# Performance work log

Hardware: AMD Instinct MI355X
Metric: run time of the kernel (lower is better)

## Reference

```python
import jax, jax.numpy as jnp
import numpy as np

S, O, J, B = 16, 8, 32, 4096
HID, OUT_HID = 240, 512
P1, P2 = 0.5, 0.65  # Bayesian (concrete) dropout probabilities, mid of [0.5, 0.8]


def setup_inputs() -> dict:
    key = jax.random.key(0)
    ks = jax.random.split(key, 20)
    sc = 0.05
    return {
        "y_t": jax.random.normal(ks[0], (B, O), jnp.float32),
        "x_filtered_prev": jax.random.normal(ks[1], (B, S), jnp.float32),
        "F": jax.random.normal(ks[2], (S, S), jnp.float32) * sc,
        "H": jax.random.normal(ks[3], (O, S), jnp.float32) * sc,
        "W_fc_in": jax.random.normal(ks[4], (HID, 2 * S + 2 * O), jnp.float32) * sc,
        "b_fc_in": jax.random.normal(ks[5], (HID,), jnp.float32) * sc,
        "W_ih": jax.random.normal(ks[6], (3 * HID, HID), jnp.float32) * sc,
        "W_hh": jax.random.normal(ks[7], (3 * HID, HID), jnp.float32) * sc,
        "b_ih": jax.random.normal(ks[8], (3 * HID,), jnp.float32) * sc,
        "b_hh": jax.random.normal(ks[9], (3 * HID,), jnp.float32) * sc,
        "W_out1": jax.random.normal(ks[10], (OUT_HID, HID), jnp.float32) * sc,
        "b_out1": jax.random.normal(ks[11], (OUT_HID,), jnp.float32) * sc,
        "W_out2": jax.random.normal(ks[12], (S * O, OUT_HID), jnp.float32) * sc,
        "b_out2": jax.random.normal(ks[13], (S * O,), jnp.float32) * sc,
        "h_init": jax.random.normal(ks[14], (HID,), jnp.float32),
        "u1": jax.random.uniform(ks[15], (J, B, HID), jnp.float32),
        "u2": jax.random.uniform(ks[16], (J, B, OUT_HID), jnp.float32),
    }


def reference(y_t, x_filtered_prev, F, H, W_fc_in, b_fc_in, W_ih, W_hh, b_ih,
              b_hh, W_out1, b_out1, W_out2, b_out2, h_init, u1, u2):
    # --- first step of step_StateBayesianKalmanNet, fully batched over (J, B) ---
    x_pred = x_filtered_prev @ F.T                 # f(x): [B,S]
    y_pred = x_pred @ H.T                          # h(x): [B,O]
    state_inno = x_filtered_prev - x_pred          # x_filt_prev - x_pred_prev
    innovation = y_t - y_pred
    diff_state = jnp.zeros_like(x_filtered_prev)   # first step: x_prev - x_prev_prev = 0
    diff_obs = y_t - y_pred                        # y_prev = h(x_pred) on first step

    feats = jnp.concatenate([state_inno, innovation, diff_state, diff_obs], -1)  # [B,48]
    x_in = jax.nn.relu(feats @ W_fc_in.T + b_fc_in)                              # [B,HID]
    mask1 = (u1 > P1).astype(x_in.dtype) / (1.0 - P1)                            # [J,B,HID]
    x_in = x_in[None] * mask1                                                    # Bayesian dropout sample j

    # single GRU cell step (torch gate order r,z,n), h_prev = h_init broadcast
    gx = x_in @ W_ih.T + b_ih                                                    # [J,B,3H]
    gh = h_init @ W_hh.T + b_hh                                                  # [3H]
    xr, xz, xn = jnp.split(gx, 3, axis=-1)
    hr, hz, hn = jnp.split(gh, 3, axis=-1)
    r = jax.nn.sigmoid(xr + hr)
    z = jax.nn.sigmoid(xz + hz)
    n = jnp.tanh(xn + r * hn)
    h_new = (1.0 - z) * n + z * h_init                                           # [J,B,HID]

    o1 = jax.nn.relu(h_new @ W_out1.T + b_out1)                                  # [J,B,OUT_HID]
    mask2 = (u2 > P2).astype(o1.dtype) / (1.0 - P2)
    o1 = o1 * mask2
    K_vec = o1 @ W_out2.T + b_out2                                               # [J,B,S*O]
    K = K_vec.reshape(J, B, S, O)

    correction = jnp.einsum('jbso,bo->jbs', K, innovation)
    x_filt = x_pred[None] + correction                                           # [J,B,S]
    ensemble = jnp.transpose(x_filt, (1, 0, 2))                                  # [B,J,S]
    final_x = ensemble.mean(axis=1)
    final_P_diag = ensemble.var(axis=1, ddof=1)                                  # torch unbiased var

    # concrete-dropout regularization (entropy of the two dropout gates, mean over J)
    reg = -(P1 * jnp.log(P1) + (1 - P1) * jnp.log(1 - P1)) \
          - (P2 * jnp.log(P2) + (1 - P2) * jnp.log(1 - P2))
    reg = jnp.asarray(reg, final_x.dtype)

    return final_x, final_P_diag, reg, ensemble
```

## Files before the change

kernel.cpp:

```cpp
#include <hip/hip_runtime.h>
#include <hip/hip_bf16.h>
#include <math.h>

#define S_DIM 16
#define O_DIM 8
#define J_DIM 32
#define B_DIM 4096
#define HID 240
#define OHID 512

typedef __attribute__((ext_vector_type(8))) short bf16x8;
typedef __attribute__((ext_vector_type(4))) float f32x4;
#define MFMA16(a,b,c) __builtin_amdgcn_mfma_f32_16x16x32_bf16((a),(b),(c),0,0,0)

#define WS_XPRED   0
#define WS_INNO    (WS_XPRED + B_DIM*S_DIM)
#define WS_FEATS   (WS_INNO + B_DIM*O_DIM)
#define WS_XIN0    (WS_FEATS + B_DIM*48)
#define WS_GH      (WS_XIN0 + B_DIM*HID)
#define WS_WB_OFF  ((WS_GH + 960) * 4)

#define OUT_X      0
#define OUT_P      (B_DIM*S_DIM)
#define OUT_REG    (2*B_DIM*S_DIM)
#define OUT_ENS    (2*B_DIM*S_DIM + 1)

__global__ void k_aux_pre(const float* __restrict__ W_ih, const float* __restrict__ W_hh,
                          const float* __restrict__ b_ih, const float* __restrict__ b_hh,
                          const float* __restrict__ h_init,
                          const float* __restrict__ W_o1, const float* __restrict__ W_o2,
                          __hip_bfloat16* __restrict__ Wihb, __hip_bfloat16* __restrict__ Wo1b,
                          __hip_bfloat16* __restrict__ Wo2b, float* __restrict__ ghb,
                          const float* __restrict__ y, const float* __restrict__ xprev,
                          const float* __restrict__ F, const float* __restrict__ Hm,
                          float* __restrict__ x_pred, float* __restrict__ inno,
                          float* __restrict__ feats)
{
    __shared__ float sF[256], sH[128];
    const int tid = threadIdx.x;
    if (blockIdx.x < 1536) {
        int t = blockIdx.x * 256 + tid;
        if (t < 768*256) {
            int n = t >> 8, k = t & 255;
            float v = (n < 720 && k < 240) ? W_ih[n*240 + k] : 0.0f;
            Wihb[t] = __float2bfloat16(v);
        } else if (t < 768*256 + 512*256) {
            int u = t - 768*256;
            int n = u >> 8, k = u & 255;
            float v = (k < 240) ? W_o1[n*240 + k] : 0.0f;
            Wo1b[u] = __float2bfloat16(v);
        } else if (t < 768*256 + 512*256 + 128*512) {
            int u = t - 768*256 - 512*256;
            Wo2b[u] = __float2bfloat16(W_o2[u]);
        }
        if (t < 720) {
            float a = b_hh[t];
            const float* wr = W_hh + t*240;
            for (int k = 0; k < 240; k++) a = fmaf(h_init[k], wr[k], a);
            if (t < 480) {
                ghb[t] = b_ih[t] + a;
            } else {
                ghb[t] = b_ih[t];
                ghb[t + 240] = a;
            }
        }
        return;
    }
    sF[tid] = F[tid];
    if (tid < 128) sH[tid] = Hm[tid];
    __syncthreads();
    int b = (blockIdx.x - 1536) * 256 + tid;
    float xf[16], xp[16], inn[8];
    #pragma unroll
    for (int s = 0; s < 16; s++) xf[s] = xprev[b*16 + s];
    #pragma unroll
    for (int s = 0; s < 16; s++) {
        float a = 0.f;
        #pragma unroll
        for (int k = 0; k < 16; k++) a = fmaf(xf[k], sF[s*16 + k], a);
        xp[s] = a;
    }
    #pragma unroll
    for (int o = 0; o < 8; o++) {
        float a = 0.f;
        #pragma unroll
        for (int k = 0; k < 16; k++) a = fmaf(xp[k], sH[o*16 + k], a);
        inn[o] = y[b*8 + o] - a;
    }
    #pragma unroll
    for (int s = 0; s < 16; s++) x_pred[b*16 + s] = xp[s];
    #pragma unroll
    for (int o = 0; o < 8; o++) inno[b*8 + o] = inn[o];
    float* fb = feats + b*48;
    #pragma unroll
    for (int s = 0; s < 16; s++) fb[s] = xf[s] - xp[s];
    #pragma unroll
    for (int o = 0; o < 8; o++) fb[16 + o] = inn[o];
    #pragma unroll
    for (int s = 0; s < 16; s++) fb[24 + s] = 0.f;
    #pragma unroll
    for (int o = 0; o < 8; o++) fb[40 + o] = inn[o];
}

__global__ void k_pre_b(const float* __restrict__ feats, const float* __restrict__ Wfc,
                        const float* __restrict__ bfc, float* __restrict__ x_in0)
{
    int t = blockIdx.x * 256 + threadIdx.x;
    int b = t / 240, h = t - b*240;
    const float* fb = feats + b*48;
    const float* wr = Wfc + h*48;
    float a = bfc[h];
    #pragma unroll
    for (int k = 0; k < 48; k += 4) {
        const float4 f4 = *(const float4*)&fb[k];
        const float4 w4 = *(const float4*)&wr[k];
        a = fmaf(f4.x, w4.x, fmaf(f4.y, w4.y, fmaf(f4.z, w4.z, fmaf(f4.w, w4.w, a))));
    }
    x_in0[t] = fmaxf(a, 0.f);
}

#define XS_STRIDE 264
#define O1_STRIDE 520

__global__ __launch_bounds__(256, 4) void k_main(
    const float* __restrict__ x_in0, const float* __restrict__ u1,
    const float* __restrict__ u2,
    const __hip_bfloat16* __restrict__ Wihb, const float* __restrict__ ghb,
    const float* __restrict__ h_init,
    const __hip_bfloat16* __restrict__ Wo1b, const float* __restrict__ b_out1,
    const __hip_bfloat16* __restrict__ Wo2b, const float* __restrict__ b_out2,
    const float* __restrict__ x_pred, const float* __restrict__ inno,
    float* __restrict__ ens)
{
    __shared__ __align__(16) char smem[38912];
    __hip_bfloat16* Xs  = (__hip_bfloat16*)smem;
    __hip_bfloat16* Hs  = (__hip_bfloat16*)(smem + 16896);
    __hip_bfloat16* O1s = (__hip_bfloat16*)smem;
    unsigned int* Mbits = (unsigned int*)(smem + 33792);
    float* XPs   = (float*)(smem + 35840);
    float* InnoS = (float*)(smem + 37888);

    const int tid = threadIdx.x;
    const int j  = blockIdx.x >> 7;
    const int b0 = (blockIdx.x & 127) << 5;

    {
        const float4* u2t = (const float4*)(u2 + ((size_t)(j*B_DIM + b0) << 9));
        const int sh = (tid & 7) * 4;
        #pragma unroll
        for (int it = 0; it < 16; ++it) {
            float4 q = u2t[tid + 256*it];
            unsigned int nib = (q.x > 0.65f ? 1u : 0u) | (q.y > 0.65f ? 2u : 0u)
                             | (q.z > 0.65f ? 4u : 0u) | (q.w > 0.65f ? 8u : 0u);
            unsigned int v = nib << sh;
            v |= __shfl_xor(v, 1);
            v |= __shfl_xor(v, 2);
            v |= __shfl_xor(v, 4);
            if ((tid & 7) == 0) Mbits[(tid >> 3) + 32*it] = v;
        }
    }

    {
        const float4* xt = (const float4*)(x_in0 + b0*240);
        const float4* ut = (const float4*)(u1 + (size_t)(j*B_DIM + b0)*240);
        #pragma unroll
        for (int it = 0; it < 8; ++it) {
            int idx = tid + 256*it;
            if (idx < 1920) {
                float4 xv = xt[idx];
                float4 uv = ut[idx];
                int flat = idx * 4;
                int i = flat / 240;
                int h = flat - i*240;
                __hip_bfloat16 o[4];
                o[0] = __float2bfloat16(uv.x > 0.5f ? 2.0f*xv.x : 0.0f);
                o[1] = __float2bfloat16(uv.y > 0.5f ? 2.0f*xv.y : 0.0f);
                o[2] = __float2bfloat16(uv.z > 0.5f ? 2.0f*xv.z : 0.0f);
                o[3] = __float2bfloat16(uv.w > 0.5f ? 2.0f*xv.w : 0.0f);
                *(uint2*)&Xs[i*XS_STRIDE + h] = *(const uint2*)o;
            }
        }
    }
    if (tid < 128) {
        int row = tid >> 2, c = 240 + ((tid & 3) << 2);
        uint2 z = {0u, 0u};
        *(uint2*)&Xs[row*XS_STRIDE + c] = z;
        *(uint2*)&Hs[row*XS_STRIDE + c] = z;
    }
    XPs[tid]       = x_pred[b0*16 + tid];
    XPs[tid + 256] = x_pred[b0*16 + tid + 256];
    InnoS[tid]     = inno[b0*8 + tid];
    __syncthreads();

    const int wave = tid >> 6;
    const int l15  = tid & 15;
    const int quad = (tid >> 4) & 3;
    const f32x4 zero4 = {0.f, 0.f, 0.f, 0.f};

    #pragma unroll 1
    for (int it = 0; it < 4; ++it) {
        f32x4 aR[2], aZ[2], aN[2];
        #pragma unroll
        for (int m = 0; m < 2; ++m) { aR[m] = zero4; aZ[m] = zero4; aN[m] = zero4; }

        const int nrow = (wave + 4*it)*16 + l15;
        const __hip_bfloat16* wr = Wihb + nrow*256;
        #pragma unroll
        for (int ks = 0; ks < 8; ++ks) {
            const int ko = ks*32 + quad*8;
            bf16x8 a0 = *(const bf16x8*)&Xs[l15*XS_STRIDE + ko];
            bf16x8 a1 = *(const bf16x8*)&Xs[(16 + l15)*XS_STRIDE + ko];
            bf16x8 br = *(const bf16x8*)&wr[ko];
            bf16x8 bz = *(const bf16x8*)&wr[240*256 + ko];
            bf16x8 bn = *(const bf16x8*)&wr[480*256 + ko];
            aR[0] = MFMA16(a0, br, aR[0]);
            aR[1] = MFMA16(a1, br, aR[1]);
            aZ[0] = MFMA16(a0, bz, aZ[0]);
            aZ[1] = MFMA16(a1, bz, aZ[1]);
            aN[0] = MFMA16(a0, bn, aN[0]);
            aN[1] = MFMA16(a1, bn, aN[1]);
        }
        const int t = wave + 4*it;
        if (t < 15) {
            const int h = t*16 + l15;
            const float add_r = ghb[h],       add_z = ghb[240 + h];
            const float add_n = ghb[480 + h], mul_n = ghb[720 + h];
            const float hi = h_init[h];
            #pragma unroll
            for (int m = 0; m < 2; ++m)
                #pragma unroll
                for (int r = 0; r < 4; ++r) {
                    const int row = m*16 + quad*4 + r;
                    float rg = 1.0f/(1.0f + expf(-(aR[m][r] + add_r)));
                    float zg = 1.0f/(1.0f + expf(-(aZ[m][r] + add_z)));
                    float ng = tanhf(aN[m][r] + add_n + rg*mul_n);
                    Hs[row*XS_STRIDE + h] = __float2bfloat16((1.0f - zg)*ng + zg*hi);
                }
        }
    }
    __syncthreads();

    {
        f32x4 acc2[8][2];
        #pragma unroll
        for (int it = 0; it < 8; it++) { acc2[it][0] = zero4; acc2[it][1] = zero4; }

        #pragma unroll
        for (int ks = 0; ks < 8; ++ks) {
            const int ko = ks*32 + quad*8;
            bf16x8 a0 = *(const bf16x8*)&Hs[l15*XS_STRIDE + ko];
            bf16x8 a1 = *(const bf16x8*)&Hs[(16 + l15)*XS_STRIDE + ko];
            #pragma unroll
            for (int it = 0; it < 8; ++it) {
                const int n = (wave*8 + it)*16 + l15;
                bf16x8 b = *(const bf16x8*)&Wo1b[n*256 + ko];
                acc2[it][0] = MFMA16(a0, b, acc2[it][0]);
                acc2[it][1] = MFMA16(a1, b, acc2[it][1]);
            }
        }
        __syncthreads();
        const float inv35 = 1.0f/0.35f;
        #pragma unroll
        for (int it = 0; it < 8; ++it) {
            const int n = (wave*8 + it)*16 + l15;
            const float bb = b_out1[n];
            const int wbase = wave*4 + (it >> 1);
            const int bitpos = ((it & 1) << 4) | l15;
            #pragma unroll
            for (int m = 0; m < 2; ++m)
                #pragma unroll
                for (int r = 0; r < 4; ++r) {
                    const int row = m*16 + quad*4 + r;
                    unsigned int mw = Mbits[row*16 + wbase];
                    float o = fmaxf(acc2[it][m][r] + bb, 0.0f);
                    o = ((mw >> bitpos) & 1u) ? o*inv35 : 0.0f;
                    O1s[row*O1_STRIDE + n] = __float2bfloat16(o);
                }
        }
    }
    __syncthreads();

    {
        f32x4 acc3[2][2];
        #pragma unroll
        for (int it = 0; it < 2; ++it) {
            const int n = (wave*2 + it)*16 + l15;
            const float bo = b_out2[n];
            f32x4 v = {bo, bo, bo, bo};
            acc3[it][0] = v; acc3[it][1] = v;
        }
        #pragma unroll
        for (int ks = 0; ks < 16; ++ks) {
            const int ko = ks*32 + quad*8;
            bf16x8 a0 = *(const bf16x8*)&O1s[l15*O1_STRIDE + ko];
            bf16x8 a1 = *(const bf16x8*)&O1s[(16 + l15)*O1_STRIDE + ko];
            #pragma unroll
            for (int it = 0; it < 2; ++it) {
                const int n = (wave*2 + it)*16 + l15;
                bf16x8 b = *(const bf16x8*)&Wo2b[n*512 + ko];
                acc3[it][0] = MFMA16(a0, b, acc3[it][0]);
                acc3[it][1] = MFMA16(a1, b, acc3[it][1]);
            }
        }
        #pragma unroll
        for (int it = 0; it < 2; ++it) {
            const int n = (wave*2 + it)*16 + l15;
            const int s = n >> 3, o = n & 7;
            #pragma unroll
            for (int m = 0; m < 2; ++m)
                #pragma unroll
                for (int r = 0; r < 4; ++r) {
                    const int row = m*16 + quad*4 + r;
                    float v = acc3[it][m][r] * InnoS[row*8 + o];
                    v += __shfl_xor(v, 1);
                    v += __shfl_xor(v, 2);
                    v += __shfl_xor(v, 4);
                    if (o == 0)
                        ens[((b0 + row)*J_DIM + j)*16 + s] = XPs[row*16 + s] + v;
                }
        }
    }
}

__global__ void k_final(const float* __restrict__ ens, float* __restrict__ out)
{
    int t = blockIdx.x * 256 + threadIdx.x;
    int b = t >> 4, s = t & 15;
    float v[32];
    #pragma unroll
    for (int jj = 0; jj < 32; jj++) v[jj] = ens[(b*32 + jj)*16 + s];
    float m = 0.f;
    #pragma unroll
    for (int jj = 0; jj < 32; jj++) m += v[jj];
    m *= (1.0f/32.0f);
    float var = 0.f;
    #pragma unroll
    for (int jj = 0; jj < 32; jj++) { float d = v[jj] - m; var = fmaf(d, d, var); }
    var *= (1.0f/31.0f);
    out[OUT_X + t] = m;
    out[OUT_P + t] = var;
    if (t == 0) out[OUT_REG] = 1.3405938195945778f;
}

extern "C" void kernel_launch(void* const* d_in, const int* in_sizes, int n_in,
                              void* d_out, int out_size, void* d_ws, size_t ws_size,
                              hipStream_t stream)
{
    (void)in_sizes; (void)n_in; (void)out_size; (void)ws_size;
    const float* y_t    = (const float*)d_in[0];
    const float* xprev  = (const float*)d_in[1];
    const float* F      = (const float*)d_in[2];
    const float* Hm     = (const float*)d_in[3];
    const float* Wfc    = (const float*)d_in[4];
    const float* bfc    = (const float*)d_in[5];
    const float* W_ih   = (const float*)d_in[6];
    const float* W_hh   = (const float*)d_in[7];
    const float* b_ih   = (const float*)d_in[8];
    const float* b_hh   = (const float*)d_in[9];
    const float* W_o1   = (const float*)d_in[10];
    const float* b_o1   = (const float*)d_in[11];
    const float* W_o2   = (const float*)d_in[12];
    const float* b_o2   = (const float*)d_in[13];
    const float* h_init = (const float*)d_in[14];
    const float* u1     = (const float*)d_in[15];
    const float* u2     = (const float*)d_in[16];

    float* out = (float*)d_out;
    float* ws  = (float*)d_ws;
    float* x_pred = ws + WS_XPRED;
    float* inno   = ws + WS_INNO;
    float* feats  = ws + WS_FEATS;
    float* x_in0  = ws + WS_XIN0;
    float* ghb    = ws + WS_GH;
    __hip_bfloat16* Wihb = (__hip_bfloat16*)((char*)d_ws + WS_WB_OFF);
    __hip_bfloat16* Wo1b = Wihb + 768*256;
    __hip_bfloat16* Wo2b = Wo1b + 512*256;
    float* ens    = out + OUT_ENS;

    k_aux_pre<<<dim3(1552), dim3(256), 0, stream>>>(W_ih, W_hh, b_ih, b_hh, h_init,
                                                    W_o1, W_o2, Wihb, Wo1b, Wo2b, ghb,
                                                    y_t, xprev, F, Hm, x_pred, inno, feats);
    k_pre_b<<<dim3(3840), dim3(256), 0, stream>>>(feats, Wfc, bfc, x_in0);
    k_main<<<dim3(4096), dim3(256), 0, stream>>>(x_in0, u1, u2, Wihb, ghb, h_init,
                                                 Wo1b, b_o1, Wo2b, b_o2,
                                                 x_pred, inno, ens);
    k_final<<<dim3(256), dim3(256), 0, stream>>>(ens, out);
}
```

Measured before the change: 843.9 us.

## Double batch tile per block to 64 rows and use fast sigmoid/tanh

Each block of 512 threads now processes 64 batch rows instead of 32. Each wave's global weight fragment loads are therefore reused across four MFMA row tiles, halving weight traffic per row. GRU gate activations switch to __expf with a hardware reciprocal. This costs double the shared memory per block and more accumulator registers, and the GRU slices are unevenly loaded across waves.

```diff
diff --git a/kernel.cpp b/kernel.cpp
--- a/kernel.cpp
+++ b/kernel.cpp
@@ -12,6 +12,15 @@
 typedef __attribute__((ext_vector_type(8))) short bf16x8;
 typedef __attribute__((ext_vector_type(4))) float f32x4;
 #define MFMA16(a,b,c) __builtin_amdgcn_mfma_f32_16x16x32_bf16((a),(b),(c),0,0,0)
+
+static __device__ __forceinline__ float fast_rcp(float x) { return __builtin_amdgcn_rcpf(x); }
+static __device__ __forceinline__ float fast_sigmoid(float x) {
+    return fast_rcp(1.0f + __expf(-x));
+}
+static __device__ __forceinline__ float fast_tanh(float x) {
+    float t = __expf(2.0f * x);
+    return 1.0f - 2.0f * fast_rcp(t + 1.0f);
+}
 
 #define WS_XPRED   0
 #define WS_INNO    (WS_XPRED + B_DIM*S_DIM)
@@ -122,7 +131,7 @@
 #define XS_STRIDE 264
 #define O1_STRIDE 520
 
-__global__ __launch_bounds__(256, 4) void k_main(
+__global__ __launch_bounds__(512, 2) void k_main(
     const float* __restrict__ x_in0, const float* __restrict__ u1,
     const float* __restrict__ u2,
     const __hip_bfloat16* __restrict__ Wihb, const float* __restrict__ ghb,
@@ -132,31 +141,31 @@
     const float* __restrict__ x_pred, const float* __restrict__ inno,
     float* __restrict__ ens)
 {
-    __shared__ __align__(16) char smem[38912];
+    __shared__ __align__(16) char smem[77824];
     __hip_bfloat16* Xs  = (__hip_bfloat16*)smem;
-    __hip_bfloat16* Hs  = (__hip_bfloat16*)(smem + 16896);
+    __hip_bfloat16* Hs  = (__hip_bfloat16*)(smem + 33792);
     __hip_bfloat16* O1s = (__hip_bfloat16*)smem;
-    unsigned int* Mbits = (unsigned int*)(smem + 33792);
-    float* XPs   = (float*)(smem + 35840);
-    float* InnoS = (float*)(smem + 37888);
+    unsigned int* Mbits = (unsigned int*)(smem + 67584);
+    float* XPs   = (float*)(smem + 71680);
+    float* InnoS = (float*)(smem + 75776);
 
     const int tid = threadIdx.x;
-    const int j  = blockIdx.x >> 7;
-    const int b0 = (blockIdx.x & 127) << 5;
+    const int j  = blockIdx.x >> 6;
+    const int b0 = (blockIdx.x & 63) << 6;
 
     {
         const float4* u2t = (const float4*)(u2 + ((size_t)(j*B_DIM + b0) << 9));
         const int sh = (tid & 7) * 4;
         #pragma unroll
         for (int it = 0; it < 16; ++it) {
-            float4 q = u2t[tid + 256*it];
+            float4 q = u2t[tid + 512*it];
             unsigned int nib = (q.x > 0.65f ? 1u : 0u) | (q.y > 0.65f ? 2u : 0u)
                              | (q.z > 0.65f ? 4u : 0u) | (q.w > 0.65f ? 8u : 0u);
             unsigned int v = nib << sh;
             v |= __shfl_xor(v, 1);
             v |= __shfl_xor(v, 2);
             v |= __shfl_xor(v, 4);
-            if ((tid & 7) == 0) Mbits[(tid >> 3) + 32*it] = v;
+            if ((tid & 7) == 0) Mbits[(tid >> 3) + 64*it] = v;
         }
     }
 
@@ -165,14 +174,13 @@
         const float4* ut = (const float4*)(u1 + (size_t)(j*B_DIM + b0)*240);
         #pragma unroll
         for (int it = 0; it < 8; ++it) {
-            int idx = tid + 256*it;
-            if (idx < 1920) {
+            int idx = tid + 512*it;
+            if (idx < 3840) {
                 float4 xv = xt[idx];
                 float4 uv = ut[idx];
-                int flat = idx * 4;
-                int i = flat / 240;
-                int h = flat - i*240;
-                __hip_bfloat16 o[4];
+                int i = idx / 60;
+                int h = (idx - i*60) * 4;
+                __align__(8) __hip_bfloat16 o[4];
                 o[0] = __float2bfloat16(uv.x > 0.5f ? 2.0f*xv.x : 0.0f);
                 o[1] = __float2bfloat16(uv.y > 0.5f ? 2.0f*xv.y : 0.0f);
                 o[2] = __float2bfloat16(uv.z > 0.5f ? 2.0f*xv.z : 0.0f);
@@ -181,15 +189,15 @@
             }
         }
     }
-    if (tid < 128) {
+    if (tid < 256) {
         int row = tid >> 2, c = 240 + ((tid & 3) << 2);
         uint2 z = {0u, 0u};
         *(uint2*)&Xs[row*XS_STRIDE + c] = z;
         *(uint2*)&Hs[row*XS_STRIDE + c] = z;
     }
     XPs[tid]       = x_pred[b0*16 + tid];
-    XPs[tid + 256] = x_pred[b0*16 + tid + 256];
-    InnoS[tid]     = inno[b0*8 + tid];
+    XPs[tid + 512] = x_pred[b0*16 + tid + 512];
+    InnoS[tid & 511] = inno[b0*8 + (tid & 511)];
     __syncthreads();
 
     const int wave = tid >> 6;
@@ -198,76 +206,83 @@
     const f32x4 zero4 = {0.f, 0.f, 0.f, 0.f};
 
     #pragma unroll 1
-    for (int it = 0; it < 4; ++it) {
-        f32x4 aR[2], aZ[2], aN[2];
-        #pragma unroll
-        for (int m = 0; m < 2; ++m) { aR[m] = zero4; aZ[m] = zero4; aN[m] = zero4; }
-
-        const int nrow = (wave + 4*it)*16 + l15;
-        const __hip_bfloat16* wr = Wihb + nrow*256;
-        #pragma unroll
-        for (int ks = 0; ks < 8; ++ks) {
-            const int ko = ks*32 + quad*8;
-            bf16x8 a0 = *(const bf16x8*)&Xs[l15*XS_STRIDE + ko];
-            bf16x8 a1 = *(const bf16x8*)&Xs[(16 + l15)*XS_STRIDE + ko];
-            bf16x8 br = *(const bf16x8*)&wr[ko];
-            bf16x8 bz = *(const bf16x8*)&wr[240*256 + ko];
-            bf16x8 bn = *(const bf16x8*)&wr[480*256 + ko];
-            aR[0] = MFMA16(a0, br, aR[0]);
-            aR[1] = MFMA16(a1, br, aR[1]);
-            aZ[0] = MFMA16(a0, bz, aZ[0]);
-            aZ[1] = MFMA16(a1, bz, aZ[1]);
-            aN[0] = MFMA16(a0, bn, aN[0]);
-            aN[1] = MFMA16(a1, bn, aN[1]);
-        }
-        const int t = wave + 4*it;
+    for (int sl = 0; sl < 2; ++sl) {
+        const int t = wave + 8*sl;
         if (t < 15) {
+            f32x4 aR[4], aZ[4], aN[4];
+            #pragma unroll
+            for (int m = 0; m < 4; ++m) { aR[m] = zero4; aZ[m] = zero4; aN[m] = zero4; }
+
+            const int nrow = t*16 + l15;
+            const __hip_bfloat16* wr = Wihb + nrow*256;
+            #pragma unroll
+            for (int ks = 0; ks < 8; ++ks) {
+                const int ko = ks*32 + quad*8;
+                bf16x8 a[4];
+                #pragma unroll
+                for (int m = 0; m < 4; ++m)
+                    a[m] = *(const bf16x8*)&Xs[(m*16 + l15)*XS_STRIDE + ko];
+                bf16x8 br = *(const bf16x8*)&wr[ko];
+                bf16x8 bz = *(const bf16x8*)&wr[240*256 + ko];
+                bf16x8 bn = *(const bf16x8*)&wr[480*256 + ko];
+                #pragma unroll
+                for (int m = 0; m < 4; ++m) {
+                    aR[m] = MFMA16(a[m], br, aR[m]);
+                    aZ[m] = MFMA16(a[m], bz, aZ[m]);
+                    aN[m] = MFMA16(a[m], bn, aN[m]);
+                }
+            }
             const int h = t*16 + l15;
             const float add_r = ghb[h],       add_z = ghb[240 + h];
             const float add_n = ghb[480 + h], mul_n = ghb[720 + h];
             const float hi = h_init[h];
             #pragma unroll
-            for (int m = 0; m < 2; ++m)
+            for (int m = 0; m < 4; ++m)
                 #pragma unroll
                 for (int r = 0; r < 4; ++r) {
                     const int row = m*16 + quad*4 + r;
-                    float rg = 1.0f/(1.0f + expf(-(aR[m][r] + add_r)));
-                    float zg = 1.0f/(1.0f + expf(-(aZ[m][r] + add_z)));
-                    float ng = tanhf(aN[m][r] + add_n + rg*mul_n);
-                    Hs[row*XS_STRIDE + h] = __float2bfloat16((1.0f - zg)*ng + zg*hi);
+                    float rg = fast_sigmoid(aR[m][r] + add_r);
+                    float zg = fast_sigmoid(aZ[m][r] + add_z);
+                    float ng = fast_tanh(aN[m][r] + add_n + rg*mul_n);
+                    Hs[row*XS_STRIDE + h] = __float2bfloat16(fmaf(zg, hi - ng, ng));
                 }
         }
     }
     __syncthreads();
 
     {
-        f32x4 acc2[8][2];
-        #pragma unroll
-        for (int it = 0; it < 8; it++) { acc2[it][0] = zero4; acc2[it][1] = zero4; }
+        f32x4 acc2[4][4];
+        #pragma unroll
+        for (int it = 0; it < 4; ++it)
+            #pragma unroll
+            for (int m = 0; m < 4; ++m) acc2[it][m] = zero4;
 
         #pragma unroll
         for (int ks = 0; ks < 8; ++ks) {
             const int ko = ks*32 + quad*8;
-            bf16x8 a0 = *(const bf16x8*)&Hs[l15*XS_STRIDE + ko];
-            bf16x8 a1 = *(const bf16x8*)&Hs[(16 + l15)*XS_STRIDE + ko];
-            #pragma unroll
-            for (int it = 0; it < 8; ++it) {
-                const int n = (wave*8 + it)*16 + l15;
+            bf16x8 a[4];
+            #pragma unroll
+            for (int m = 0; m < 4; ++m)
+                a[m] = *(const bf16x8*)&Hs[(m*16 + l15)*XS_STRIDE + ko];
+            #pragma unroll
+            for (int it = 0; it < 4; ++it) {
+                const int n = (wave*4 + it)*16 + l15;
                 bf16x8 b = *(const bf16x8*)&Wo1b[n*256 + ko];
-                acc2[it][0] = MFMA16(a0, b, acc2[it][0]);
-                acc2[it][1] = MFMA16(a1, b, acc2[it][1]);
+                #pragma unroll
+                for (int m = 0; m < 4; ++m)
+                    acc2[it][m] = MFMA16(a[m], b, acc2[it][m]);
             }
         }
         __syncthreads();
         const float inv35 = 1.0f/0.35f;
         #pragma unroll
-        for (int it = 0; it < 8; ++it) {
-            const int n = (wave*8 + it)*16 + l15;
+        for (int it = 0; it < 4; ++it) {
+            const int n = (wave*4 + it)*16 + l15;
             const float bb = b_out1[n];
-            const int wbase = wave*4 + (it >> 1);
+            const int wbase = (wave*4 + it) >> 1;
             const int bitpos = ((it & 1) << 4) | l15;
             #pragma unroll
-            for (int m = 0; m < 2; ++m)
+            for (int m = 0; m < 4; ++m)
                 #pragma unroll
                 for (int r = 0; r < 4; ++r) {
                     const int row = m*16 + quad*4 + r;
@@ -281,44 +296,35 @@
     __syncthreads();
 
     {
-        f32x4 acc3[2][2];
-        #pragma unroll
-        for (int it = 0; it < 2; ++it) {
-            const int n = (wave*2 + it)*16 + l15;
-            const float bo = b_out2[n];
-            f32x4 v = {bo, bo, bo, bo};
-            acc3[it][0] = v; acc3[it][1] = v;
-        }
+        const int n = wave*16 + l15;
+        const float bo = b_out2[n];
+        f32x4 acc3[4];
+        #pragma unroll
+        for (int m = 0; m < 4; ++m) { f32x4 v = {bo, bo, bo, bo}; acc3[m] = v; }
+
         #pragma unroll
         for (int ks = 0; ks < 16; ++ks) {
             const int ko = ks*32 + quad*8;
-            bf16x8 a0 = *(const bf16x8*)&O1s[l15*O1_STRIDE + ko];
-            bf16x8 a1 = *(const bf16x8*)&O1s[(16 + l15)*O1_STRIDE + ko];
-            #pragma unroll
-            for (int it = 0; it < 2; ++it) {
-                const int n = (wave*2 + it)*16 + l15;
-                bf16x8 b = *(const bf16x8*)&Wo2b[n*512 + ko];
-                acc3[it][0] = MFMA16(a0, b, acc3[it][0]);
-                acc3[it][1] = MFMA16(a1, b, acc3[it][1]);
-            }
-        }
-        #pragma unroll
-        for (int it = 0; it < 2; ++it) {
-            const int n = (wave*2 + it)*16 + l15;
-            const int s = n >> 3, o = n & 7;
-            #pragma unroll
-            for (int m = 0; m < 2; ++m)
-                #pragma unroll
-                for (int r = 0; r < 4; ++r) {
-                    const int row = m*16 + quad*4 + r;
-                    float v = acc3[it][m][r] * InnoS[row*8 + o];
-                    v += __shfl_xor(v, 1);
-                    v += __shfl_xor(v, 2);
-                    v += __shfl_xor(v, 4);
-                    if (o == 0)
-                        ens[((b0 + row)*J_DIM + j)*16 + s] = XPs[row*16 + s] + v;
-                }
-        }
+            bf16x8 b = *(const bf16x8*)&Wo2b[n*512 + ko];
+            #pragma unroll
+            for (int m = 0; m < 4; ++m) {
+                bf16x8 a = *(const bf16x8*)&O1s[(m*16 + l15)*O1_STRIDE + ko];
+                acc3[m] = MFMA16(a, b, acc3[m]);
+            }
+        }
+        const int s = n >> 3, o = n & 7;
+        #pragma unroll
+        for (int m = 0; m < 4; ++m)
+            #pragma unroll
+            for (int r = 0; r < 4; ++r) {
+                const int row = m*16 + quad*4 + r;
+                float v = acc3[m][r] * InnoS[row*8 + o];
+                v += __shfl_xor(v, 1);
+                v += __shfl_xor(v, 2);
+                v += __shfl_xor(v, 4);
+                if (o == 0)
+                    ens[((b0 + row)*J_DIM + j)*16 + s] = XPs[row*16 + s] + v;
+            }
     }
 }
 
@@ -381,7 +387,7 @@
                                                     W_o1, W_o2, Wihb, Wo1b, Wo2b, ghb,
                                                     y_t, xprev, F, Hm, x_pred, inno, feats);
     k_pre_b<<<dim3(3840), dim3(256), 0, stream>>>(feats, Wfc, bfc, x_in0);
-    k_main<<<dim3(4096), dim3(256), 0, stream>>>(x_in0, u1, u2, Wihb, ghb, h_init,
+    k_main<<<dim3(2048), dim3(512), 0, stream>>>(x_in0, u1, u2, Wihb, ghb, h_init,
                                                  Wo1b, b_o1, Wo2b, b_o2,
                                                  x_pred, inno, ens);
     k_final<<<dim3(256), dim3(256), 0, stream>>>(ens, out);
```

New measurement: 770.3 us. -8.7%, faster.
